# Kernel optimization log

Hardware: AMD Instinct MI355X
Metric: run time of the kernel (lower is better)

Reference implementation:

```python
import jax, jax.numpy as jnp
import numpy as np


def _lstm_scan(x, w_ih, w_hh, b_ih, b_hh):
    """Unidirectional LSTM, PyTorch gate order (i, f, g, o).
    x: [B, T, C]; w_ih: [4H, C]; w_hh: [4H, H]. Returns [B, T, H]."""
    H = w_hh.shape[1]
    # Precompute input contribution for all timesteps (one big GEMM).
    xg = jnp.einsum('btc,gc->btg', x, w_ih) + b_ih + b_hh  # [B, T, 4H]

    def step(carry, xg_t):
        h, c = carry
        gates = xg_t + h @ w_hh.T
        i, f, g, o = jnp.split(gates, 4, axis=-1)
        c = jax.nn.sigmoid(f) * c + jax.nn.sigmoid(i) * jnp.tanh(g)
        h = jax.nn.sigmoid(o) * jnp.tanh(c)
        return (h, c), h

    B = x.shape[0]
    h0 = jnp.zeros((B, H), x.dtype)
    _, hs = jax.lax.scan(step, (h0, h0), jnp.swapaxes(xg, 0, 1))
    return jnp.swapaxes(hs, 0, 1)  # [B, T, H]


def _bilstm(x, w_ih_f, w_hh_f, b_ih_f, b_hh_f, w_ih_b, w_hh_b, b_ih_b, b_hh_b):
    fwd = _lstm_scan(x, w_ih_f, w_hh_f, b_ih_f, b_hh_f)
    bwd = _lstm_scan(x[:, ::-1], w_ih_b, w_hh_b, b_ih_b, b_hh_b)[:, ::-1]
    return jnp.concatenate([fwd, bwd], axis=-1)  # [B, T, 2H]


def setup_inputs() -> dict:
    key = jax.random.key(0)
    B, Hh, Ww, C, Hd = 64, 48, 48, 192, 48
    ks = jax.random.split(key, 20)
    s = 1.0 / np.sqrt(Hd)  # PyTorch LSTM init scale
    inp = {"x": jax.random.normal(ks[0], (B, Hh, Ww, C), jnp.float32)}
    names = ["v_w_ih_f", "v_w_hh_f", "v_b_ih_f", "v_b_hh_f",
             "v_w_ih_b", "v_w_hh_b", "v_b_ih_b", "v_b_hh_b",
             "h_w_ih_f", "h_w_hh_f", "h_b_ih_f", "h_b_hh_f",
             "h_w_ih_b", "h_w_hh_b", "h_b_ih_b", "h_b_hh_b"]
    shapes = [(4 * Hd, C), (4 * Hd, Hd), (4 * Hd,), (4 * Hd,)] * 4
    for i, (n, sh) in enumerate(zip(names, shapes)):
        inp[n] = jax.random.uniform(ks[1 + i], sh, jnp.float32, -s, s)
    inp["proj_w"] = jax.random.uniform(ks[17], (C, 4 * Hd), jnp.float32, -s, s)
    inp["proj_b"] = jax.random.uniform(ks[18], (C,), jnp.float32, -s, s)
    return inp


def reference(x, v_w_ih_f, v_w_hh_f, v_b_ih_f, v_b_hh_f,
              v_w_ih_b, v_w_hh_b, v_b_ih_b, v_b_hh_b,
              h_w_ih_f, h_w_hh_f, h_b_ih_f, h_b_hh_f,
              h_w_ih_b, h_w_hh_b, h_b_ih_b, h_b_hh_b,
              proj_w, proj_b):
    B, Hh, Ww, C = x.shape
    # Vertical: scan over height for each column.
    xv = jnp.transpose(x, (0, 2, 1, 3)).reshape(B * Ww, Hh, C)
    v = _bilstm(xv, v_w_ih_f, v_w_hh_f, v_b_ih_f, v_b_hh_f,
                v_w_ih_b, v_w_hh_b, v_b_ih_b, v_b_hh_b)
    v = jnp.transpose(v.reshape(B, Ww, Hh, -1), (0, 2, 1, 3))  # [B,H,W,2Hd]
    # Horizontal: scan over width for each row.
    xh = x.reshape(B * Hh, Ww, C)
    h = _bilstm(xh, h_w_ih_f, h_w_hh_f, h_b_ih_f, h_b_hh_f,
                h_w_ih_b, h_w_hh_b, h_b_ih_b, h_b_hh_b)
    h = h.reshape(B, Hh, Ww, -1)  # [B,H,W,2Hd]
    combined = jnp.concatenate([v, h], axis=-1)  # [B,H,W,4Hd]
    return jnp.einsum('bhwk,ck->bhwc', combined, proj_w) + proj_b
```

## Files before the change

### kernel.cpp

```cpp
#include <hip/hip_runtime.h>

typedef short short8 __attribute__((ext_vector_type(8)));
typedef short short4v __attribute__((ext_vector_type(4)));
typedef float f32x4 __attribute__((ext_vector_type(4)));
typedef unsigned short u16;

__device__ __forceinline__ u16 f2bf(float f) {
  unsigned int u = __builtin_bit_cast(unsigned int, f);
  u = (u + 0x7FFFu + ((u >> 16) & 1u)) >> 16;
  return (u16)u;
}
__device__ __forceinline__ short8 cvt8(float4 a, float4 b) {
  short8 v;
  v[0] = (short)f2bf(a.x); v[1] = (short)f2bf(a.y);
  v[2] = (short)f2bf(a.z); v[3] = (short)f2bf(a.w);
  v[4] = (short)f2bf(b.x); v[5] = (short)f2bf(b.y);
  v[6] = (short)f2bf(b.z); v[7] = (short)f2bf(b.w);
  return v;
}
__device__ __forceinline__ short8 cvt8s(float4 a, float4 b, float s) {
  short8 v;
  v[0] = (short)f2bf(a.x * s); v[1] = (short)f2bf(a.y * s);
  v[2] = (short)f2bf(a.z * s); v[3] = (short)f2bf(a.w * s);
  v[4] = (short)f2bf(b.x * s); v[5] = (short)f2bf(b.y * s);
  v[6] = (short)f2bf(b.z * s); v[7] = (short)f2bf(b.w * s);
  return v;
}

#define NPX 147456
#define L2E 1.44269504088896f

__global__ __launch_bounds__(256)
void xcvt_kernel(const float* __restrict__ x, u16* __restrict__ xbf)
{
  size_t c = ((size_t)blockIdx.x * 256 + threadIdx.x) * 8;
  const float4* p = (const float4*)(x + c);
  *(short8*)(xbf + c) = cvt8(p[0], p[1]);
}

__global__ __launch_bounds__(192)
void fused_scan_kernel(const u16* __restrict__ xbf,
    const float* __restrict__ wi0, const float* __restrict__ wi1,
    const float* __restrict__ wi2, const float* __restrict__ wi3,
    const float* __restrict__ u0, const float* __restrict__ u1,
    const float* __restrict__ u2, const float* __restrict__ u3,
    const float* __restrict__ bi0, const float* __restrict__ bh0,
    const float* __restrict__ bi1, const float* __restrict__ bh1,
    const float* __restrict__ bi2, const float* __restrict__ bh2,
    const float* __restrict__ bi3, const float* __restrict__ bh3,
    u16* __restrict__ comb)
{
  __shared__ u16 hl[2][1152];
  const int tid  = threadIdx.x;
  const int lane = tid & 63;
  const int wv   = tid >> 6;
  const int cl   = lane & 15;
  const int kg   = lane >> 4;
  const int W    = blockIdx.x;
  const int dir  = W / 192;
  const int g    = W - dir * 192;
  const int bb   = g / 3;
  const int rc   = (g - bb * 3) * 16 + cl;
  const bool vert = dir < 2;
  const bool bwd  = (dir & 1) != 0;

  const float* wp  = dir == 0 ? wi0 : dir == 1 ? wi1 : dir == 2 ? wi2 : wi3;
  const float* up  = dir == 0 ? u0  : dir == 1 ? u1  : dir == 2 ? u2  : u3;
  const float* bip = dir == 0 ? bi0 : dir == 1 ? bi1 : dir == 2 ? bi2 : bi3;
  const float* bhp = dir == 0 ? bh0 : dir == 1 ? bh1 : dir == 2 ? bh2 : bh3;

  const int tp0 = bwd ? 47 : 0;
  const int dpx = (vert ? 48 : 1) * (bwd ? -1 : 1);
  const int px0 = vert ? (bb * 48 + tp0) * 48 + rc : (bb * 48 + rc) * 48 + tp0;

  const u16* xp = xbf + (size_t)px0 * 192 + kg * 8;
  const ptrdiff_t xstep = (ptrdiff_t)dpx * 192;

  short8 xf[6];
  #pragma unroll
  for (int kk = 0; kk < 6; ++kk) xf[kk] = *(const short8*)(xp + kk * 32);

  short8 wf[4][6], uf[4][2];
  f32x4 bv[4];
  #pragma unroll
  for (int q = 0; q < 4; ++q) {
    const float sc = (q == 2) ? 2.0f * L2E : L2E;
    int n = q * 48 + wv * 16 + cl;
    #pragma unroll
    for (int kk = 0; kk < 6; ++kk) {
      const float4* p = (const float4*)(wp + n * 192 + kk * 32 + kg * 8);
      wf[q][kk] = cvt8s(p[0], p[1], sc);
    }
    {
      const float4* p = (const float4*)(up + n * 48 + kg * 8);
      uf[q][0] = cvt8s(p[0], p[1], sc);
    }
    if (kg < 2) {
      const float4* p = (const float4*)(up + n * 48 + 32 + kg * 8);
      uf[q][1] = cvt8s(p[0], p[1], sc);
    } else {
      short8 z = {}; uf[q][1] = z;
    }
    #pragma unroll
    for (int r = 0; r < 4; ++r) {
      int nb = q * 48 + wv * 16 + kg * 4 + r;
      bv[q][r] = (bip[nb] + bhp[nb]) * sc;
    }
  }

  for (int i = tid; i < 2304; i += 192) (&hl[0][0])[i] = 0;
  __syncthreads();

  f32x4 pA[4], pB[4];
  #pragma unroll
  for (int q = 0; q < 4; ++q) pA[q] = bv[q];
  #pragma unroll
  for (int kk = 0; kk < 6; ++kk)
    #pragma unroll
    for (int q = 0; q < 4; ++q)
      pA[q] = __builtin_amdgcn_mfma_f32_16x16x32_bf16(wf[q][kk], xf[kk], pA[q], 0, 0, 0);
  xp += xstep;
  #pragma unroll
  for (int kk = 0; kk < 6; ++kk) xf[kk] = *(const short8*)(xp + kk * 32);

  float c[4] = {0.f, 0.f, 0.f, 0.f};
  int hcur = 0;
  u16* cbp = comb + (size_t)dir * NPX * 48 + (size_t)px0 * 48 + wv * 16 + kg * 4;
  const ptrdiff_t cstep = (ptrdiff_t)dpx * 48;

  auto STEP = [&](f32x4 (&cur)[4], f32x4 (&nxt)[4], int t) {
    short8 hb0 = *(const short8*)&hl[hcur][cl * 72 + kg * 8];
    short8 hb1 = *(const short8*)&hl[hcur][cl * 72 + 32 + kg * 8];

    if (t < 47) {
      #pragma unroll
      for (int q = 0; q < 4; ++q) nxt[q] = bv[q];
      #pragma unroll
      for (int kk = 0; kk < 6; ++kk)
        #pragma unroll
        for (int q = 0; q < 4; ++q)
          nxt[q] = __builtin_amdgcn_mfma_f32_16x16x32_bf16(wf[q][kk], xf[kk], nxt[q], 0, 0, 0);
      if (t < 46) {
        xp += xstep;
        #pragma unroll
        for (int kk = 0; kk < 6; ++kk) xf[kk] = *(const short8*)(xp + kk * 32);
      }
    }

    #pragma unroll
    for (int q = 0; q < 4; ++q)
      cur[q] = __builtin_amdgcn_mfma_f32_16x16x32_bf16(uf[q][0], hb0, cur[q], 0, 0, 0);
    #pragma unroll
    for (int q = 0; q < 4; ++q)
      cur[q] = __builtin_amdgcn_mfma_f32_16x16x32_bf16(uf[q][1], hb1, cur[q], 0, 0, 0);

    short4v h4;
    #pragma unroll
    for (int r = 0; r < 4; ++r) {
      float ii = __builtin_amdgcn_rcpf(1.0f + __builtin_exp2f(-cur[0][r]));
      float ff = __builtin_amdgcn_rcpf(1.0f + __builtin_exp2f(-cur[1][r]));
      float gg = 1.0f - 2.0f * __builtin_amdgcn_rcpf(1.0f + __builtin_exp2f(cur[2][r]));
      float oo = __builtin_amdgcn_rcpf(1.0f + __builtin_exp2f(-cur[3][r]));
      float cc = ff * c[r] + ii * gg;
      c[r] = cc;
      float th = 1.0f - 2.0f * __builtin_amdgcn_rcpf(1.0f + __builtin_exp2f(cc * (2.0f * L2E)));
      h4[r] = (short)f2bf(oo * th);
    }
    *(short4v*)&hl[hcur ^ 1][cl * 72 + wv * 16 + kg * 4] = h4;
    *(short4v*)cbp = h4;
    cbp += cstep;
    __syncthreads();
    hcur ^= 1;
  };

  for (int it = 0; it < 24; ++it) {
    STEP(pA, pB, 2 * it);
    STEP(pB, pA, 2 * it + 1);
  }
}

__global__ __launch_bounds__(256)
void proj_kernel(const u16* __restrict__ comb,
                 const float* __restrict__ pw,
                 const float* __restrict__ pb,
                 float* __restrict__ out)
{
  __shared__ u16 al[12288];
  const int tid  = threadIdx.x;
  const int lane = tid & 63;
  const int wv   = tid >> 6;
  const int cl   = lane & 15;
  const int kg   = lane >> 4;
  const int pxb  = blockIdx.x * 64;

  #pragma unroll
  for (int i = 0; i < 6; ++i) {
    int ch = tid + 256 * i;
    int pxl = ch / 24;
    int kk0 = (ch % 24) << 3;
    int d   = kk0 / 48;
    short8 v = *(const short8*)(comb + ((size_t)d * NPX + pxb + pxl) * 48 + (kk0 - d * 48));
    *(short8*)&al[(pxl * 192 + kk0) ^ ((pxl & 7) << 3)] = v;
  }

  short8 wf[3][6];
  #pragma unroll
  for (int nt = 0; nt < 3; ++nt) {
    int n = wv * 48 + nt * 16 + cl;
    #pragma unroll
    for (int kk = 0; kk < 6; ++kk) {
      const float4* p = (const float4*)(pw + n * 192 + kk * 32 + kg * 8);
      wf[nt][kk] = cvt8(p[0], p[1]);
    }
  }
  f32x4 bvv[3];
  #pragma unroll
  for (int nt = 0; nt < 3; ++nt)
    #pragma unroll
    for (int r = 0; r < 4; ++r)
      bvv[nt][r] = pb[wv * 48 + nt * 16 + kg * 4 + r];

  __syncthreads();

  f32x4 acc[3][4];
  #pragma unroll
  for (int nt = 0; nt < 3; ++nt)
    #pragma unroll
    for (int mi = 0; mi < 4; ++mi) acc[nt][mi] = bvv[nt];

  #pragma unroll
  for (int kk = 0; kk < 6; ++kk) {
    short8 bfr[4];
    #pragma unroll
    for (int mi = 0; mi < 4; ++mi) {
      int row = mi * 16 + cl;
      bfr[mi] = *(const short8*)&al[(row * 192 + kk * 32 + kg * 8) ^ ((row & 7) << 3)];
    }
    #pragma unroll
    for (int nt = 0; nt < 3; ++nt)
      #pragma unroll
      for (int mi = 0; mi < 4; ++mi)
        acc[nt][mi] = __builtin_amdgcn_mfma_f32_16x16x32_bf16(wf[nt][kk], bfr[mi], acc[nt][mi], 0, 0, 0);
  }

  #pragma unroll
  for (int nt = 0; nt < 3; ++nt)
    #pragma unroll
    for (int mi = 0; mi < 4; ++mi) {
      size_t o = (size_t)(pxb + mi * 16 + cl) * 192 + wv * 48 + nt * 16 + kg * 4;
      *(f32x4*)(out + o) = acc[nt][mi];
    }
}

extern "C" void kernel_launch(void* const* d_in, const int* in_sizes, int n_in,
                              void* d_out, int out_size, void* d_ws, size_t ws_size,
                              hipStream_t stream) {
  const float* x = (const float*)d_in[0];
  u16* xbf  = (u16*)d_ws;
  u16* comb = (u16*)d_ws + (size_t)NPX * 192;

  xcvt_kernel<<<13824, 256, 0, stream>>>(x, xbf);

  fused_scan_kernel<<<768, 192, 0, stream>>>(
      xbf,
      (const float*)d_in[1], (const float*)d_in[5],
      (const float*)d_in[9], (const float*)d_in[13],
      (const float*)d_in[2], (const float*)d_in[6],
      (const float*)d_in[10], (const float*)d_in[14],
      (const float*)d_in[3],  (const float*)d_in[4],
      (const float*)d_in[7],  (const float*)d_in[8],
      (const float*)d_in[11], (const float*)d_in[12],
      (const float*)d_in[15], (const float*)d_in[16],
      comb);

  proj_kernel<<<2304, 256, 0, stream>>>(
      comb, (const float*)d_in[17], (const float*)d_in[18], (float*)d_out);
}
```

Baseline: 228.8 us.

## Give each wave its own sequence group with shared-LDS input weights, no block barrier

```diff
diff --git a/kernel.cpp b/kernel.cpp
--- a/kernel.cpp
+++ b/kernel.cpp
@@ -50,28 +50,67 @@
     const float* __restrict__ bi3, const float* __restrict__ bh3,
     u16* __restrict__ comb)
 {
-  __shared__ u16 hl[2][1152];
+  __shared__ u16 wl[36864];
+  __shared__ u16 hs[3][1152];
+
   const int tid  = threadIdx.x;
   const int lane = tid & 63;
   const int wv   = tid >> 6;
   const int cl   = lane & 15;
   const int kg   = lane >> 4;
-  const int W    = blockIdx.x;
-  const int dir  = W / 192;
-  const int g    = W - dir * 192;
-  const int bb   = g / 3;
-  const int rc   = (g - bb * 3) * 16 + cl;
-  const bool vert = dir < 2;
-  const bool bwd  = (dir & 1) != 0;
+  const int dir  = blockIdx.x >> 6;
+  const int sub  = blockIdx.x & 63;
 
   const float* wp  = dir == 0 ? wi0 : dir == 1 ? wi1 : dir == 2 ? wi2 : wi3;
   const float* up  = dir == 0 ? u0  : dir == 1 ? u1  : dir == 2 ? u2  : u3;
   const float* bip = dir == 0 ? bi0 : dir == 1 ? bi1 : dir == 2 ? bi2 : bi3;
   const float* bhp = dir == 0 ? bh0 : dir == 1 ? bh1 : dir == 2 ? bh2 : bh3;
 
-  const int tp0 = bwd ? 47 : 0;
-  const int dpx = (vert ? 48 : 1) * (bwd ? -1 : 1);
-  const int px0 = vert ? (bb * 48 + tp0) * 48 + rc : (bb * 48 + rc) * 48 + tp0;
+  for (int i = 0; i < 24; ++i) {
+    int ch  = tid + 192 * i;
+    int row = ch / 24;
+    int k0  = (ch % 24) * 8;
+    float sc = (row >= 96 && row < 144) ? 2.0f * L2E : L2E;
+    const float4* p = (const float4*)(wp + row * 192 + k0);
+    *(short8*)&wl[(row * 192 + k0) ^ ((row & 7) << 3)] = cvt8s(p[0], p[1], sc);
+  }
+
+  short8 uf[12][2];
+  #pragma unroll
+  for (int nt = 0; nt < 12; ++nt) {
+    int n = nt * 16 + cl;
+    float sc = (n >= 96 && n < 144) ? 2.0f * L2E : L2E;
+    {
+      const float4* p = (const float4*)(up + n * 48 + kg * 8);
+      uf[nt][0] = cvt8s(p[0], p[1], sc);
+    }
+    if (kg < 2) {
+      const float4* p = (const float4*)(up + n * 48 + 32 + kg * 8);
+      uf[nt][1] = cvt8s(p[0], p[1], sc);
+    } else if (kg == 2) {
+      short8 v = {};
+      v[0] = (short)f2bf((bip[n] + bhp[n]) * sc);
+      uf[nt][1] = v;
+    } else {
+      short8 z = {}; uf[nt][1] = z;
+    }
+  }
+
+  #pragma unroll
+  for (int i = 0; i < 18; ++i) {
+    int idx = lane * 18 + i;
+    hs[wv][idx] = (idx % 72 == 48) ? (u16)0x3F80 : (u16)0;
+  }
+  __syncthreads();
+
+  const int W    = sub * 3 + wv;
+  const int bb   = W / 3;
+  const int rc   = (W - bb * 3) * 16 + cl;
+  const bool vert = dir < 2;
+  const bool bwd  = (dir & 1) != 0;
+  const int tp0  = bwd ? 47 : 0;
+  const int dpx  = (vert ? 48 : 1) * (bwd ? -1 : 1);
+  const int px0  = vert ? (bb * 48 + tp0) * 48 + rc : (bb * 48 + rc) * 48 + tp0;
 
   const u16* xp = xbf + (size_t)px0 * 192 + kg * 8;
   const ptrdiff_t xstep = (ptrdiff_t)dpx * 192;
@@ -80,102 +119,69 @@
   #pragma unroll
   for (int kk = 0; kk < 6; ++kk) xf[kk] = *(const short8*)(xp + kk * 32);
 
-  short8 wf[4][6], uf[4][2];
-  f32x4 bv[4];
-  #pragma unroll
-  for (int q = 0; q < 4; ++q) {
-    const float sc = (q == 2) ? 2.0f * L2E : L2E;
-    int n = q * 48 + wv * 16 + cl;
+  f32x4 c0 = {0.f,0.f,0.f,0.f}, c1 = c0, c2 = c0;
+  u16* cbp = comb + ((size_t)dir * NPX + px0) * 48 + kg * 4;
+  const ptrdiff_t cstep = (ptrdiff_t)dpx * 48;
+
+  const int swz = (cl & 7) << 3;
+
+  for (int t = 0; t < 48; ++t) {
+    short8 hb0 = *(const short8*)&hs[wv][cl * 72 + kg * 8];
+    short8 hb1 = *(const short8*)&hs[wv][cl * 72 + 32 + kg * 8];
+
+    f32x4 acc[12];
+    #pragma unroll
+    for (int nt = 0; nt < 12; ++nt) acc[nt] = (f32x4){0.f,0.f,0.f,0.f};
+
     #pragma unroll
     for (int kk = 0; kk < 6; ++kk) {
-      const float4* p = (const float4*)(wp + n * 192 + kk * 32 + kg * 8);
-      wf[q][kk] = cvt8s(p[0], p[1], sc);
-    }
-    {
-      const float4* p = (const float4*)(up + n * 48 + kg * 8);
-      uf[q][0] = cvt8s(p[0], p[1], sc);
-    }
-    if (kg < 2) {
-      const float4* p = (const float4*)(up + n * 48 + 32 + kg * 8);
-      uf[q][1] = cvt8s(p[0], p[1], sc);
-    } else {
-      short8 z = {}; uf[q][1] = z;
-    }
-    #pragma unroll
-    for (int r = 0; r < 4; ++r) {
-      int nb = q * 48 + wv * 16 + kg * 4 + r;
-      bv[q][r] = (bip[nb] + bhp[nb]) * sc;
-    }
-  }
-
-  for (int i = tid; i < 2304; i += 192) (&hl[0][0])[i] = 0;
-  __syncthreads();
-
-  f32x4 pA[4], pB[4];
-  #pragma unroll
-  for (int q = 0; q < 4; ++q) pA[q] = bv[q];
-  #pragma unroll
-  for (int kk = 0; kk < 6; ++kk)
-    #pragma unroll
-    for (int q = 0; q < 4; ++q)
-      pA[q] = __builtin_amdgcn_mfma_f32_16x16x32_bf16(wf[q][kk], xf[kk], pA[q], 0, 0, 0);
-  xp += xstep;
-  #pragma unroll
-  for (int kk = 0; kk < 6; ++kk) xf[kk] = *(const short8*)(xp + kk * 32);
-
-  float c[4] = {0.f, 0.f, 0.f, 0.f};
-  int hcur = 0;
-  u16* cbp = comb + (size_t)dir * NPX * 48 + (size_t)px0 * 48 + wv * 16 + kg * 4;
-  const ptrdiff_t cstep = (ptrdiff_t)dpx * 48;
-
-  auto STEP = [&](f32x4 (&cur)[4], f32x4 (&nxt)[4], int t) {
-    short8 hb0 = *(const short8*)&hl[hcur][cl * 72 + kg * 8];
-    short8 hb1 = *(const short8*)&hl[hcur][cl * 72 + 32 + kg * 8];
+      short8 w[6];
+      #pragma unroll
+      for (int nt = 0; nt < 6; ++nt)
+        w[nt] = *(const short8*)&wl[((nt * 16 + cl) * 192 + kk * 32 + kg * 8) ^ swz];
+      #pragma unroll
+      for (int nt = 0; nt < 6; ++nt)
+        acc[nt] = __builtin_amdgcn_mfma_f32_16x16x32_bf16(w[nt], xf[kk], acc[nt], 0, 0, 0);
+      #pragma unroll
+      for (int nt = 0; nt < 6; ++nt)
+        w[nt] = *(const short8*)&wl[(((nt + 6) * 16 + cl) * 192 + kk * 32 + kg * 8) ^ swz];
+      #pragma unroll
+      for (int nt = 0; nt < 6; ++nt)
+        acc[nt + 6] = __builtin_amdgcn_mfma_f32_16x16x32_bf16(w[nt], xf[kk], acc[nt + 6], 0, 0, 0);
+    }
 
     if (t < 47) {
-      #pragma unroll
-      for (int q = 0; q < 4; ++q) nxt[q] = bv[q];
-      #pragma unroll
-      for (int kk = 0; kk < 6; ++kk)
-        #pragma unroll
-        for (int q = 0; q < 4; ++q)
-          nxt[q] = __builtin_amdgcn_mfma_f32_16x16x32_bf16(wf[q][kk], xf[kk], nxt[q], 0, 0, 0);
-      if (t < 46) {
-        xp += xstep;
-        #pragma unroll
-        for (int kk = 0; kk < 6; ++kk) xf[kk] = *(const short8*)(xp + kk * 32);
+      xp += xstep;
+      #pragma unroll
+      for (int kk = 0; kk < 6; ++kk) xf[kk] = *(const short8*)(xp + kk * 32);
+    }
+
+    #pragma unroll
+    for (int nt = 0; nt < 12; ++nt)
+      acc[nt] = __builtin_amdgcn_mfma_f32_16x16x32_bf16(uf[nt][0], hb0, acc[nt], 0, 0, 0);
+    #pragma unroll
+    for (int nt = 0; nt < 12; ++nt)
+      acc[nt] = __builtin_amdgcn_mfma_f32_16x16x32_bf16(uf[nt][1], hb1, acc[nt], 0, 0, 0);
+
+    #pragma unroll
+    for (int q = 0; q < 3; ++q) {
+      f32x4& cq = q == 0 ? c0 : q == 1 ? c1 : c2;
+      short4v h4;
+      #pragma unroll
+      for (int r = 0; r < 4; ++r) {
+        float ii = __builtin_amdgcn_rcpf(1.0f + __builtin_exp2f(-acc[q][r]));
+        float ff = __builtin_amdgcn_rcpf(1.0f + __builtin_exp2f(-acc[3 + q][r]));
+        float gg = 1.0f - 2.0f * __builtin_amdgcn_rcpf(1.0f + __builtin_exp2f(acc[6 + q][r]));
+        float oo = __builtin_amdgcn_rcpf(1.0f + __builtin_exp2f(-acc[9 + q][r]));
+        float cc = ff * cq[r] + ii * gg;
+        cq[r] = cc;
+        float th = 1.0f - 2.0f * __builtin_amdgcn_rcpf(1.0f + __builtin_exp2f(cc * (2.0f * L2E)));
+        h4[r] = (short)f2bf(oo * th);
       }
-    }
-
-    #pragma unroll
-    for (int q = 0; q < 4; ++q)
-      cur[q] = __builtin_amdgcn_mfma_f32_16x16x32_bf16(uf[q][0], hb0, cur[q], 0, 0, 0);
-    #pragma unroll
-    for (int q = 0; q < 4; ++q)
-      cur[q] = __builtin_amdgcn_mfma_f32_16x16x32_bf16(uf[q][1], hb1, cur[q], 0, 0, 0);
-
-    short4v h4;
-    #pragma unroll
-    for (int r = 0; r < 4; ++r) {
-      float ii = __builtin_amdgcn_rcpf(1.0f + __builtin_exp2f(-cur[0][r]));
-      float ff = __builtin_amdgcn_rcpf(1.0f + __builtin_exp2f(-cur[1][r]));
-      float gg = 1.0f - 2.0f * __builtin_amdgcn_rcpf(1.0f + __builtin_exp2f(cur[2][r]));
-      float oo = __builtin_amdgcn_rcpf(1.0f + __builtin_exp2f(-cur[3][r]));
-      float cc = ff * c[r] + ii * gg;
-      c[r] = cc;
-      float th = 1.0f - 2.0f * __builtin_amdgcn_rcpf(1.0f + __builtin_exp2f(cc * (2.0f * L2E)));
-      h4[r] = (short)f2bf(oo * th);
-    }
-    *(short4v*)&hl[hcur ^ 1][cl * 72 + wv * 16 + kg * 4] = h4;
-    *(short4v*)cbp = h4;
+      *(short4v*)&hs[wv][cl * 72 + q * 16 + kg * 4] = h4;
+      *(short4v*)(cbp + q * 16) = h4;
+    }
     cbp += cstep;
-    __syncthreads();
-    hcur ^= 1;
-  };
-
-  for (int it = 0; it < 24; ++it) {
-    STEP(pA, pB, 2 * it);
-    STEP(pB, pA, 2 * it + 1);
   }
 }
 
@@ -261,7 +267,7 @@
 
   xcvt_kernel<<<13824, 256, 0, stream>>>(x, xbf);
 
-  fused_scan_kernel<<<768, 192, 0, stream>>>(
+  fused_scan_kernel<<<256, 192, 0, stream>>>(
       xbf,
       (const float*)d_in[1], (const float*)d_in[5],
       (const float*)d_in[9], (const float*)d_in[13],
```

Measured after the change: 256.7 us. 12.2% more time.

## Pack three scan chains per block with shared-LDS input weights and bias folding

Applied to the files above, without the earlier changes.

```diff
diff --git a/kernel.cpp b/kernel.cpp
--- a/kernel.cpp
+++ b/kernel.cpp
@@ -38,7 +38,7 @@
   *(short8*)(xbf + c) = cvt8(p[0], p[1]);
 }
 
-__global__ __launch_bounds__(192)
+__global__ __launch_bounds__(576)
 void fused_scan_kernel(const u16* __restrict__ xbf,
     const float* __restrict__ wi0, const float* __restrict__ wi1,
     const float* __restrict__ wi2, const float* __restrict__ wi3,
@@ -50,17 +50,21 @@
     const float* __restrict__ bi3, const float* __restrict__ bh3,
     u16* __restrict__ comb)
 {
-  __shared__ u16 hl[2][1152];
-  const int tid  = threadIdx.x;
-  const int lane = tid & 63;
-  const int wv   = tid >> 6;
-  const int cl   = lane & 15;
-  const int kg   = lane >> 4;
-  const int W    = blockIdx.x;
-  const int dir  = W / 192;
-  const int g    = W - dir * 192;
-  const int bb   = g / 3;
-  const int rc   = (g - bb * 3) * 16 + cl;
+  __shared__ u16 wl[36864];
+  __shared__ u16 hs[3][2][1152];
+
+  const int tid   = threadIdx.x;
+  const int chain = tid / 192;
+  const int ctid  = tid - chain * 192;
+  const int lane  = ctid & 63;
+  const int wv    = ctid >> 6;
+  const int cl    = lane & 15;
+  const int kg    = lane >> 4;
+  const int dir   = blockIdx.x >> 6;
+  const int W     = blockIdx.x * 3 + chain;
+  const int g     = W - dir * 192;
+  const int bb    = g / 3;
+  const int rc    = (g - bb * 3) * 16 + cl;
   const bool vert = dir < 2;
   const bool bwd  = (dir & 1) != 0;
 
@@ -69,28 +73,40 @@
   const float* bip = dir == 0 ? bi0 : dir == 1 ? bi1 : dir == 2 ? bi2 : bi3;
   const float* bhp = dir == 0 ? bh0 : dir == 1 ? bh1 : dir == 2 ? bh2 : bh3;
 
+  for (int i = 0; i < 8; ++i) {
+    int ch  = tid + 576 * i;
+    int row = ch / 24;
+    int k0  = (ch % 24) * 8;
+    float sc = (row >= 96 && row < 144) ? 2.0f * L2E : L2E;
+    const float4* p = (const float4*)(wp + row * 192 + k0);
+    *(short8*)&wl[(row * 192 + k0) ^ ((row & 7) << 3)] = cvt8s(p[0], p[1], sc);
+  }
+
   const int tp0 = bwd ? 47 : 0;
   const int dpx = (vert ? 48 : 1) * (bwd ? -1 : 1);
   const int px0 = vert ? (bb * 48 + tp0) * 48 + rc : (bb * 48 + rc) * 48 + tp0;
 
   const u16* xp = xbf + (size_t)px0 * 192 + kg * 8;
   const ptrdiff_t xstep = (ptrdiff_t)dpx * 192;
-
   short8 xf[6];
   #pragma unroll
   for (int kk = 0; kk < 6; ++kk) xf[kk] = *(const short8*)(xp + kk * 32);
 
-  short8 wf[4][6], uf[4][2];
-  f32x4 bv[4];
+  short8 wfr[2][6];
+  #pragma unroll
+  for (int q = 0; q < 2; ++q) {
+    int n = q * 48 + wv * 16 + cl;
+    #pragma unroll
+    for (int kk = 0; kk < 6; ++kk) {
+      const float4* p = (const float4*)(wp + n * 192 + kk * 32 + kg * 8);
+      wfr[q][kk] = cvt8s(p[0], p[1], L2E);
+    }
+  }
+  short8 uf[4][2];
   #pragma unroll
   for (int q = 0; q < 4; ++q) {
     const float sc = (q == 2) ? 2.0f * L2E : L2E;
     int n = q * 48 + wv * 16 + cl;
-    #pragma unroll
-    for (int kk = 0; kk < 6; ++kk) {
-      const float4* p = (const float4*)(wp + n * 192 + kk * 32 + kg * 8);
-      wf[q][kk] = cvt8s(p[0], p[1], sc);
-    }
     {
       const float4* p = (const float4*)(up + n * 48 + kg * 8);
       uf[q][0] = cvt8s(p[0], p[1], sc);
@@ -98,84 +114,75 @@
     if (kg < 2) {
       const float4* p = (const float4*)(up + n * 48 + 32 + kg * 8);
       uf[q][1] = cvt8s(p[0], p[1], sc);
+    } else if (kg == 2) {
+      short8 v = {};
+      v[0] = (short)f2bf((bip[n] + bhp[n]) * sc);
+      uf[q][1] = v;
     } else {
       short8 z = {}; uf[q][1] = z;
     }
+  }
+
+  for (int i = ctid; i < 2304; i += 192)
+    (&hs[chain][0][0])[i] = (i % 72 == 48) ? (u16)0x3F80 : (u16)0;
+  __syncthreads();
+
+  f32x4 c = {0.f, 0.f, 0.f, 0.f};
+  int hcur = 0;
+  u16* cbp = comb + ((size_t)dir * NPX + px0) * 48 + wv * 16 + kg * 4;
+  const ptrdiff_t cstep = (ptrdiff_t)dpx * 48;
+  const int swz = (cl & 7) << 3;
+  const int r2 = (96 + wv * 16 + cl) * 192 + kg * 8;
+  const int r3 = (144 + wv * 16 + cl) * 192 + kg * 8;
+
+  for (int t = 0; t < 48; ++t) {
+    short8 hb0 = *(const short8*)&hs[chain][hcur][cl * 72 + kg * 8];
+    short8 hb1 = *(const short8*)&hs[chain][hcur][cl * 72 + 32 + kg * 8];
+
+    f32x4 acc[4];
+    #pragma unroll
+    for (int q = 0; q < 4; ++q) acc[q] = (f32x4){0.f, 0.f, 0.f, 0.f};
+
+    #pragma unroll
+    for (int kk = 0; kk < 6; ++kk) {
+      acc[0] = __builtin_amdgcn_mfma_f32_16x16x32_bf16(wfr[0][kk], xf[kk], acc[0], 0, 0, 0);
+      acc[1] = __builtin_amdgcn_mfma_f32_16x16x32_bf16(wfr[1][kk], xf[kk], acc[1], 0, 0, 0);
+      short8 w2 = *(const short8*)&wl[(r2 + kk * 32) ^ swz];
+      short8 w3 = *(const short8*)&wl[(r3 + kk * 32) ^ swz];
+      acc[2] = __builtin_amdgcn_mfma_f32_16x16x32_bf16(w2, xf[kk], acc[2], 0, 0, 0);
+      acc[3] = __builtin_amdgcn_mfma_f32_16x16x32_bf16(w3, xf[kk], acc[3], 0, 0, 0);
+    }
+
+    if (t < 47) {
+      xp += xstep;
+      #pragma unroll
+      for (int kk = 0; kk < 6; ++kk) xf[kk] = *(const short8*)(xp + kk * 32);
+    }
+
+    #pragma unroll
+    for (int q = 0; q < 4; ++q)
+      acc[q] = __builtin_amdgcn_mfma_f32_16x16x32_bf16(uf[q][0], hb0, acc[q], 0, 0, 0);
+    #pragma unroll
+    for (int q = 0; q < 4; ++q)
+      acc[q] = __builtin_amdgcn_mfma_f32_16x16x32_bf16(uf[q][1], hb1, acc[q], 0, 0, 0);
+
+    short4v h4;
     #pragma unroll
     for (int r = 0; r < 4; ++r) {
-      int nb = q * 48 + wv * 16 + kg * 4 + r;
-      bv[q][r] = (bip[nb] + bhp[nb]) * sc;
-    }
-  }
-
-  for (int i = tid; i < 2304; i += 192) (&hl[0][0])[i] = 0;
-  __syncthreads();
-
-  f32x4 pA[4], pB[4];
-  #pragma unroll
-  for (int q = 0; q < 4; ++q) pA[q] = bv[q];
-  #pragma unroll
-  for (int kk = 0; kk < 6; ++kk)
-    #pragma unroll
-    for (int q = 0; q < 4; ++q)
-      pA[q] = __builtin_amdgcn_mfma_f32_16x16x32_bf16(wf[q][kk], xf[kk], pA[q], 0, 0, 0);
-  xp += xstep;
-  #pragma unroll
-  for (int kk = 0; kk < 6; ++kk) xf[kk] = *(const short8*)(xp + kk * 32);
-
-  float c[4] = {0.f, 0.f, 0.f, 0.f};
-  int hcur = 0;
-  u16* cbp = comb + (size_t)dir * NPX * 48 + (size_t)px0 * 48 + wv * 16 + kg * 4;
-  const ptrdiff_t cstep = (ptrdiff_t)dpx * 48;
-
-  auto STEP = [&](f32x4 (&cur)[4], f32x4 (&nxt)[4], int t) {
-    short8 hb0 = *(const short8*)&hl[hcur][cl * 72 + kg * 8];
-    short8 hb1 = *(const short8*)&hl[hcur][cl * 72 + 32 + kg * 8];
-
-    if (t < 47) {
-      #pragma unroll
-      for (int q = 0; q < 4; ++q) nxt[q] = bv[q];
-      #pragma unroll
-      for (int kk = 0; kk < 6; ++kk)
-        #pragma unroll
-        for (int q = 0; q < 4; ++q)
-          nxt[q] = __builtin_amdgcn_mfma_f32_16x16x32_bf16(wf[q][kk], xf[kk], nxt[q], 0, 0, 0);
-      if (t < 46) {
-        xp += xstep;
-        #pragma unroll
-        for (int kk = 0; kk < 6; ++kk) xf[kk] = *(const short8*)(xp + kk * 32);
-      }
-    }
-
-    #pragma unroll
-    for (int q = 0; q < 4; ++q)
-      cur[q] = __builtin_amdgcn_mfma_f32_16x16x32_bf16(uf[q][0], hb0, cur[q], 0, 0, 0);
-    #pragma unroll
-    for (int q = 0; q < 4; ++q)
-      cur[q] = __builtin_amdgcn_mfma_f32_16x16x32_bf16(uf[q][1], hb1, cur[q], 0, 0, 0);
-
-    short4v h4;
-    #pragma unroll
-    for (int r = 0; r < 4; ++r) {
-      float ii = __builtin_amdgcn_rcpf(1.0f + __builtin_exp2f(-cur[0][r]));
-      float ff = __builtin_amdgcn_rcpf(1.0f + __builtin_exp2f(-cur[1][r]));
-      float gg = 1.0f - 2.0f * __builtin_amdgcn_rcpf(1.0f + __builtin_exp2f(cur[2][r]));
-      float oo = __builtin_amdgcn_rcpf(1.0f + __builtin_exp2f(-cur[3][r]));
+      float ii = __builtin_amdgcn_rcpf(1.0f + __builtin_exp2f(-acc[0][r]));
+      float ff = __builtin_amdgcn_rcpf(1.0f + __builtin_exp2f(-acc[1][r]));
+      float gg = 1.0f - 2.0f * __builtin_amdgcn_rcpf(1.0f + __builtin_exp2f(acc[2][r]));
+      float oo = __builtin_amdgcn_rcpf(1.0f + __builtin_exp2f(-acc[3][r]));
       float cc = ff * c[r] + ii * gg;
       c[r] = cc;
       float th = 1.0f - 2.0f * __builtin_amdgcn_rcpf(1.0f + __builtin_exp2f(cc * (2.0f * L2E)));
       h4[r] = (short)f2bf(oo * th);
     }
-    *(short4v*)&hl[hcur ^ 1][cl * 72 + wv * 16 + kg * 4] = h4;
+    *(short4v*)&hs[chain][hcur ^ 1][cl * 72 + wv * 16 + kg * 4] = h4;
     *(short4v*)cbp = h4;
     cbp += cstep;
     __syncthreads();
     hcur ^= 1;
-  };
-
-  for (int it = 0; it < 24; ++it) {
-    STEP(pA, pB, 2 * it);
-    STEP(pB, pA, 2 * it + 1);
   }
 }
 
@@ -261,7 +268,7 @@
 
   xcvt_kernel<<<13824, 256, 0, stream>>>(x, xbf);
 
-  fused_scan_kernel<<<768, 192, 0, stream>>>(
+  fused_scan_kernel<<<256, 576, 0, stream>>>(
       xbf,
       (const float*)d_in[1], (const float*)d_in[5],
       (const float*)d_in[9], (const float*)d_in[13],
```

Measured after the change: 211.1 us. 7.7% less time.
